# Performance work log

Hardware: AMD Instinct MI355X
Metric: run time of the kernel (lower is better)

## Reference

```python
import jax, jax.numpy as jnp
import numpy as np

H = 16  # num_attention_heads

def setup_inputs() -> dict:
    key = jax.random.key(0)
    ks = jax.random.split(key, 4)
    B, S, D = 4, 2048, 1024
    scale = 1.0 / np.sqrt(D)
    return {
        "hidden_states": jax.random.normal(ks[0], (B, S, D), dtype=jnp.float32),
        "attention_mask": jnp.zeros((B, 1, 1, S), dtype=jnp.float32),
        "Wq": jax.random.normal(ks[1], (D, D), dtype=jnp.float32) * scale,
        "bq": jnp.zeros((D,), dtype=jnp.float32),
        "Wk": jax.random.normal(ks[2], (D, D), dtype=jnp.float32) * scale,
        "bk": jnp.zeros((D,), dtype=jnp.float32),
        "Wv": jax.random.normal(ks[3], (D, D), dtype=jnp.float32) * scale,
        "bv": jnp.zeros((D,), dtype=jnp.float32),
    }

def _split_heads(x, B, S):
    # [B,S,D] -> [B,H,S,Dh]
    return x.reshape(B, S, H, -1).transpose(0, 2, 1, 3)

def reference(hidden_states, attention_mask, Wq, bq, Wk, bk, Wv, bv):
    B, S, D = hidden_states.shape
    Dh = D // H
    q = _split_heads(hidden_states @ Wq.T + bq, B, S)  # [B,H,S,Dh]
    k = _split_heads(hidden_states @ Wk.T + bk, B, S)
    v = _split_heads(hidden_states @ Wv.T + bv, B, S)
    scores = jnp.einsum("bhqd,bhkd->bhqk", q, k) / jnp.sqrt(jnp.float32(Dh))
    scores = scores + attention_mask  # additive mask, broadcast [B,1,1,S]
    probs = jax.nn.softmax(scores, axis=-1)  # dropout is identity in eval mode
    ctx = jnp.einsum("bhqk,bhkd->bhqd", probs, v)  # [B,H,S,Dh]
    ctx = ctx.transpose(0, 2, 1, 3).reshape(B, S, D)
    return ctx
```

## Files before the change

kernel.cpp:

```cpp
#include <hip/hip_runtime.h>
#include <hip/hip_bf16.h>
#include <stdint.h>

#define LOG2E 1.44269504088896340736f
#define SCL   (0.125f * LOG2E)

typedef __attribute__((ext_vector_type(8)))  short short8;
typedef __attribute__((ext_vector_type(4)))  float floatx4;
typedef __attribute__((ext_vector_type(16))) float floatx16;
typedef __attribute__((ext_vector_type(4)))  unsigned short ushort4v;

#define GLP(g, l)                                                              \
    __builtin_amdgcn_global_load_lds(                                          \
        (const __attribute__((address_space(1))) void*)(g),                    \
        (__attribute__((address_space(3))) void*)(l), 16, 0, 0)

#if __has_builtin(__builtin_amdgcn_exp2f)
#define EXP2(x) __builtin_amdgcn_exp2f(x)
#else
#define EXP2(x) exp2f(x)
#endif

static __device__ __forceinline__ unsigned short f2bf(float f) {
    union { float f; unsigned u; } v; v.f = f;
    unsigned r = v.u + 0x7FFFu + ((v.u >> 16) & 1u);
    return (unsigned short)(r >> 16);
}

static __device__ __forceinline__ unsigned pack2bf(float a, float b) {
    __hip_bfloat162 h = __float22bfloat162_rn(make_float2(a, b));
    union { __hip_bfloat162 h; unsigned u; } c; c.h = h; return c.u;
}

__global__ __launch_bounds__(256) void cvt_kernel(const float* __restrict__ in,
                                                  unsigned short* __restrict__ out,
                                                  int n4) {
    int i = blockIdx.x * 256 + threadIdx.x;
    if (i < n4) {
        float4 v = ((const float4*)in)[i];
        ushort4v o;
        o.x = f2bf(v.x); o.y = f2bf(v.y); o.z = f2bf(v.z); o.w = f2bf(v.w);
        ((ushort4v*)out)[i] = o;
    }
}

__global__ __launch_bounds__(256) void cvt_w3m(const float* __restrict__ Wq,
                                               const float* __restrict__ Wk,
                                               const float* __restrict__ Wv,
                                               const float* __restrict__ mask,
                                               unsigned short* __restrict__ out,
                                               float* __restrict__ maskl) {
    int i = blockIdx.x * 256 + threadIdx.x;
    if (i < 786432) {
        const float* src; int j;
        if (i < 262144)      { src = Wq; j = i; }
        else if (i < 524288) { src = Wk; j = i - 262144; }
        else                 { src = Wv; j = i - 524288; }
        float4 v = ((const float4*)src)[j];
        ushort4v o;
        o.x = f2bf(v.x); o.y = f2bf(v.y); o.z = f2bf(v.z); o.w = f2bf(v.w);
        ((ushort4v*)out)[i] = o;
    } else if (i < 786432 + 2048) {
        int j = i - 786432;
        float4 v = ((const float4*)mask)[j];
        ((float4*)maskl)[j] = make_float4(v.x * LOG2E, v.y * LOG2E,
                                          v.z * LOG2E, v.w * LOG2E);
    }
}

__global__ __launch_bounds__(256) void qkv_gemm(
        const unsigned short* __restrict__ X,
        const unsigned short* __restrict__ W,
        const float* __restrict__ bq, const float* __restrict__ bk,
        const float* __restrict__ bv,
        unsigned short* __restrict__ Qf,
        unsigned short* __restrict__ Kf,
        unsigned short* __restrict__ Vt)
{
    __shared__ __align__(16) unsigned short sh[17408];
    unsigned short* Ash = sh;
    unsigned short* Bsh = sh + 8192;

    const int tid  = threadIdx.x;
    const int lane = tid & 63;
    const int wv   = tid >> 6;
    const int quad = lane >> 4;
    const int ln   = lane & 15;
    const int mBase = blockIdx.x * 128;
    const int nBase = blockIdx.y * 128;
    const int wm = (wv >> 1) * 64;
    const int wn = (wv & 1) * 64;

    floatx4 acc[4][4];
#pragma unroll
    for (int i = 0; i < 4; ++i)
#pragma unroll
        for (int j = 0; j < 4; ++j) acc[i][j] = 0.0f;

    const int sr = lane >> 3;
    const int kc = (lane & 7) ^ sr;

    for (int kb = 0; kb < 1024; kb += 64) {
        __syncthreads();
#pragma unroll
        for (int s = 0; s < 4; ++s) {
            const int seg = wv * 4 + s;
            const int row = seg * 8 + sr;
            GLP(X + (size_t)(mBase + row) * 1024 + kb + kc * 8, Ash + seg * 512);
            GLP(W + (size_t)(nBase + row) * 1024 + kb + kc * 8, Bsh + seg * 512);
        }
        __syncthreads();
#pragma unroll
        for (int kk = 0; kk < 2; ++kk) {
            const int c = kk * 4 + quad;
            short8 aF[4], bF[4];
#pragma unroll
            for (int i = 0; i < 4; ++i) {
                const int R = wm + i * 16 + ln;
                aF[i] = *(const short8*)(Ash + (R >> 3) * 512 + (R & 7) * 64 + ((c ^ (R & 7)) * 8));
            }
#pragma unroll
            for (int j = 0; j < 4; ++j) {
                const int R = wn + j * 16 + ln;
                bF[j] = *(const short8*)(Bsh + (R >> 3) * 512 + (R & 7) * 64 + ((c ^ (R & 7)) * 8));
            }
#pragma unroll
            for (int i = 0; i < 4; ++i)
#pragma unroll
                for (int j = 0; j < 4; ++j)
                    acc[i][j] = __builtin_amdgcn_mfma_f32_16x16x32_bf16(
                        aF[i], bF[j], acc[i][j], 0, 0, 0);
        }
    }

    if (blockIdx.y < 16) {
        unsigned short* dst = (blockIdx.y < 8) ? Qf : Kf;
        const float* bias   = (blockIdx.y < 8) ? bq : bk;
        const int nb = nBase & 1023;
        float bj[4];
#pragma unroll
        for (int j = 0; j < 4; ++j)
            bj[j] = bias[nb + wn + j * 16 + ln];
        __syncthreads();
#pragma unroll
        for (int j = 0; j < 4; ++j) {
            const int col = wn + j * 16 + ln;
#pragma unroll
            for (int i = 0; i < 4; ++i) {
                const int row0 = wm + i * 16 + quad * 4;
#pragma unroll
                for (int r = 0; r < 4; ++r)
                    sh[(row0 + r) * 136 + col] = f2bf(acc[i][j][r] + bj[j]);
            }
        }
        __syncthreads();
#pragma unroll
        for (int it = 0; it < 8; ++it) {
            const int row  = it * 16 + (tid >> 4);
            const int part = tid & 15;
            short8 v = *(const short8*)(sh + row * 136 + part * 8);
            *(short8*)(dst + (size_t)(mBase + row) * 1024 + nb + part * 8) = v;
        }
    } else {
#pragma unroll
        for (int j = 0; j < 4; ++j) {
            const int gn = nBase + wn + j * 16 + ln;
            const int c  = gn & 1023;
            const int h  = c >> 6;
            const int d  = c & 63;
            const float bias = bv[c];
#pragma unroll
            for (int i = 0; i < 4; ++i) {
                const int gm0 = mBase + wm + i * 16 + quad * 4;
                const int b   = gm0 >> 11;
                const int s0  = gm0 & 2047;
                ushort4v pv;
#pragma unroll
                for (int r = 0; r < 4; ++r) pv[r] = f2bf(acc[i][j][r] + bias);
                *(ushort4v*)(Vt + (size_t)((b * 16 + h) * 64 + d) * 2048 + s0) = pv;
            }
        }
    }
}

__global__ __launch_bounds__(256) void attn_kernel(
        const unsigned short* __restrict__ Qf,
        const unsigned short* __restrict__ Kf,
        const unsigned short* __restrict__ VT,
        const float* __restrict__ maskl,
        float* __restrict__ out)
{
    __shared__ __align__(16) unsigned short Ksh[128 * 64];
    __shared__ __align__(16) unsigned short Vsh[64 * 128];
    __shared__ __align__(16) unsigned short Psh[4 * 32 * 64];
    __shared__ __align__(16) float Msh[128];

    const int tid  = threadIdx.x;
    const int lane = tid & 63;
    const int wv   = tid >> 6;
    const int q32  = lane & 31;
    const int hi   = lane >> 5;
    const int bh   = blockIdx.x & 63;
    const int qt   = blockIdx.x >> 6;
    const int b    = bh >> 4;
    const int h    = bh & 15;
    const int q0   = qt * 128 + wv * 32;
    const int sw   = q32 & 7;

    short8 bQ[4];
#pragma unroll
    for (int ks = 0; ks < 4; ++ks)
        bQ[ks] = *(const short8*)(Qf + (size_t)(b * 2048 + q0 + q32) * 1024
                                     + h * 64 + ks * 16 + hi * 8);
    short8 ones;
#pragma unroll
    for (int j = 0; j < 8; ++j) ones[j] = (short)0x3F80;

    floatx16 accO0 = 0.0f, accO1 = 0.0f, accL = 0.0f;

    const unsigned short* gK = Kf + (size_t)(b * 2048) * 1024 + h * 64;
    const unsigned short* gV = VT + (size_t)(bh * 64) * 2048;
    const float* mrow = maskl + b * 2048;
    unsigned short* pw = Psh + wv * (32 * 64);

    const int krr = lane >> 3;
    const int kcs = lane & 7;
    const int vrr = lane >> 4;
    const int vcs = lane & 15;

    for (int kb = 0; kb < 2048; kb += 128) {
        __syncthreads();
#pragma unroll
        for (int s = 0; s < 4; ++s) {
            const int seg = wv * 4 + s;
            const int rK  = seg * 8 + krr;
            const int cK  = kcs ^ (rK & 7);
            GLP(gK + (size_t)(kb + rK) * 1024 + cK * 8, Ksh + seg * 512);
            const int rV  = seg * 4 + vrr;
            const int cV  = vcs ^ (rV & 7);
            GLP(gV + (size_t)rV * 2048 + kb + cV * 8, Vsh + seg * 512);
        }
        if (tid < 32) GLP(mrow + kb + lane * 4, Msh);
        __syncthreads();

#pragma unroll
        for (int half = 0; half < 2; ++half) {
#pragma unroll
            for (int mt = 0; mt < 2; ++mt) {
                floatx16 sacc = 0.0f;
#pragma unroll
                for (int ks = 0; ks < 4; ++ks) {
                    const int row  = half * 64 + mt * 32 + q32;
                    const int slot = (2 * ks + hi) ^ sw;
                    short8 aK = *(const short8*)(Ksh + row * 64 + slot * 8);
                    sacc = __builtin_amdgcn_mfma_f32_32x32x16_bf16(aK, bQ[ks], sacc, 0, 0, 0);
                }
#pragma unroll
                for (int g = 0; g < 4; ++g) {
                    const int key0 = mt * 32 + g * 8 + hi * 4;
                    float4 mv4 = *(const float4*)(Msh + half * 64 + key0);
                    float p0 = EXP2(sacc[g * 4 + 0] * SCL + mv4.x);
                    float p1 = EXP2(sacc[g * 4 + 1] * SCL + mv4.y);
                    float p2 = EXP2(sacc[g * 4 + 2] * SCL + mv4.z);
                    float p3 = EXP2(sacc[g * 4 + 3] * SCL + mv4.w);
                    *(uint2*)(pw + q32 * 64 + (((mt * 4 + g) ^ sw) * 8) + hi * 4) =
                        make_uint2(pack2bf(p0, p1), pack2bf(p2, p3));
                }
            }

#pragma unroll
            for (int ks = 0; ks < 4; ++ks) {
                const int cs = (2 * ks + hi) ^ sw;
                short8 aP  = *(const short8*)(pw + q32 * 64 + cs * 8);
                const int cv = half * 8 + cs;
                short8 bV0 = *(const short8*)(Vsh + q32 * 128 + cv * 8);
                short8 bV1 = *(const short8*)(Vsh + (32 + q32) * 128 + cv * 8);
                accO0 = __builtin_amdgcn_mfma_f32_32x32x16_bf16(aP, bV0, accO0, 0, 0, 0);
                accO1 = __builtin_amdgcn_mfma_f32_32x32x16_bf16(aP, bV1, accO1, 0, 0, 0);
                accL  = __builtin_amdgcn_mfma_f32_32x32x16_bf16(aP, ones, accL, 0, 0, 0);
            }
        }
    }

#pragma unroll
    for (int g = 0; g < 4; ++g)
#pragma unroll
        for (int rr = 0; rr < 4; ++rr) {
            const int r   = g * 4 + rr;
            const int row = rr + 8 * g + 4 * hi;
            const float linv = 1.0f / accL[r];
            float* op = out + (size_t)(b * 2048 + q0 + row) * 1024 + h * 64 + q32;
            op[0]  = accO0[r] * linv;
            op[32] = accO1[r] * linv;
        }
}

extern "C" void kernel_launch(void* const* d_in, const int* in_sizes, int n_in,
                              void* d_out, int out_size, void* d_ws, size_t ws_size,
                              hipStream_t stream) {
    const float* X    = (const float*)d_in[0];
    const float* mask = (const float*)d_in[1];
    const float* Wq   = (const float*)d_in[2];
    const float* bq   = (const float*)d_in[3];
    const float* Wk   = (const float*)d_in[4];
    const float* bk   = (const float*)d_in[5];
    const float* Wv   = (const float*)d_in[6];
    const float* bv   = (const float*)d_in[7];
    float* out = (float*)d_out;

    char* ws = (char*)d_ws;
    unsigned short* xb  = (unsigned short*)(ws);
    unsigned short* wb  = (unsigned short*)(ws + 16777216);
    unsigned short* qf  = (unsigned short*)(ws + 23068672);
    unsigned short* kf  = (unsigned short*)(ws + 39845888);
    unsigned short* vtb = (unsigned short*)(ws + 56623104);
    float*          ml  = (float*)(ws + 73400320);

    cvt_kernel<<<8192, 256, 0, stream>>>(X, xb, 2097152);
    cvt_w3m<<<3080, 256, 0, stream>>>(Wq, Wk, Wv, mask, wb, ml);

    qkv_gemm<<<dim3(64, 24), 256, 0, stream>>>(xb, wb, bq, bk, bv, qf, kf, vtb);

    attn_kernel<<<1024, 256, 0, stream>>>(qf, kf, vtb, ml, out);
}
```

Measured before the change: 272.8 us.

## Keep softmax probabilities in registers via lane shuffles and sum row totals in VALU

The attention kernel no longer stages the bf16 probability tile through shared memory. It builds the MFMA A operand for the PV product directly from the score accumulator registers, using cross-half-wave shuffles. The row-sum MFMA against a ones vector is replaced by a scalar per-lane accumulation that is reduced at the end and passed through a small shared buffer. Launch bounds now request 4 blocks per CU to raise occupancy, which may force register pressure or spills. The row sum is now accumulated in fp32 before bf16 rounding, so it can differ slightly from the bf16-weighted numerator.

```diff
diff --git a/kernel.cpp b/kernel.cpp
--- a/kernel.cpp
+++ b/kernel.cpp
@@ -183,7 +183,7 @@
     }
 }
 
-__global__ __launch_bounds__(256) void attn_kernel(
+__global__ __launch_bounds__(256, 4) void attn_kernel(
         const unsigned short* __restrict__ Qf,
         const unsigned short* __restrict__ Kf,
         const unsigned short* __restrict__ VT,
@@ -192,8 +192,8 @@
 {
     __shared__ __align__(16) unsigned short Ksh[128 * 64];
     __shared__ __align__(16) unsigned short Vsh[64 * 128];
-    __shared__ __align__(16) unsigned short Psh[4 * 32 * 64];
     __shared__ __align__(16) float Msh[128];
+    __shared__ __align__(16) float Lsh[128];
 
     const int tid  = threadIdx.x;
     const int lane = tid & 63;
@@ -212,16 +212,13 @@
     for (int ks = 0; ks < 4; ++ks)
         bQ[ks] = *(const short8*)(Qf + (size_t)(b * 2048 + q0 + q32) * 1024
                                      + h * 64 + ks * 16 + hi * 8);
-    short8 ones;
-#pragma unroll
-    for (int j = 0; j < 8; ++j) ones[j] = (short)0x3F80;
-
-    floatx16 accO0 = 0.0f, accO1 = 0.0f, accL = 0.0f;
+
+    floatx16 accO0 = 0.0f, accO1 = 0.0f;
+    float l_c = 0.0f;
 
     const unsigned short* gK = Kf + (size_t)(b * 2048) * 1024 + h * 64;
     const unsigned short* gV = VT + (size_t)(bh * 64) * 2048;
     const float* mrow = maskl + b * 2048;
-    unsigned short* pw = Psh + wv * (32 * 64);
 
     const int krr = lane >> 3;
     const int kcs = lane & 7;
@@ -255,44 +252,56 @@
                     short8 aK = *(const short8*)(Ksh + row * 64 + slot * 8);
                     sacc = __builtin_amdgcn_mfma_f32_32x32x16_bf16(aK, bQ[ks], sacc, 0, 0, 0);
                 }
-#pragma unroll
-                for (int g = 0; g < 4; ++g) {
-                    const int key0 = mt * 32 + g * 8 + hi * 4;
-                    float4 mv4 = *(const float4*)(Msh + half * 64 + key0);
-                    float p0 = EXP2(sacc[g * 4 + 0] * SCL + mv4.x);
-                    float p1 = EXP2(sacc[g * 4 + 1] * SCL + mv4.y);
-                    float p2 = EXP2(sacc[g * 4 + 2] * SCL + mv4.z);
-                    float p3 = EXP2(sacc[g * 4 + 3] * SCL + mv4.w);
-                    *(uint2*)(pw + q32 * 64 + (((mt * 4 + g) ^ sw) * 8) + hi * 4) =
-                        make_uint2(pack2bf(p0, p1), pack2bf(p2, p3));
+                unsigned u0[4], u1[4], e0[4], e1[4];
+#pragma unroll
+                for (int a = 0; a < 4; ++a) {
+                    const int key0 = half * 64 + mt * 32 + a * 8 + hi * 4;
+                    float4 mv4 = *(const float4*)(Msh + key0);
+                    float p0 = EXP2(sacc[a * 4 + 0] * SCL + mv4.x);
+                    float p1 = EXP2(sacc[a * 4 + 1] * SCL + mv4.y);
+                    float p2 = EXP2(sacc[a * 4 + 2] * SCL + mv4.z);
+                    float p3 = EXP2(sacc[a * 4 + 3] * SCL + mv4.w);
+                    l_c += (p0 + p1) + (p2 + p3);
+                    u0[a] = pack2bf(p0, p1);
+                    u1[a] = pack2bf(p2, p3);
+                    e0[a] = (unsigned)__shfl_xor((int)u0[a], 32, 64);
+                    e1[a] = (unsigned)__shfl_xor((int)u1[a], 32, 64);
                 }
-            }
-
-#pragma unroll
-            for (int ks = 0; ks < 4; ++ks) {
-                const int cs = (2 * ks + hi) ^ sw;
-                short8 aP  = *(const short8*)(pw + q32 * 64 + cs * 8);
-                const int cv = half * 8 + cs;
-                short8 bV0 = *(const short8*)(Vsh + q32 * 128 + cv * 8);
-                short8 bV1 = *(const short8*)(Vsh + (32 + q32) * 128 + cv * 8);
-                accO0 = __builtin_amdgcn_mfma_f32_32x32x16_bf16(aP, bV0, accO0, 0, 0, 0);
-                accO1 = __builtin_amdgcn_mfma_f32_32x32x16_bf16(aP, bV1, accO1, 0, 0, 0);
-                accL  = __builtin_amdgcn_mfma_f32_32x32x16_bf16(aP, ones, accL, 0, 0, 0);
-            }
-        }
-    }
-
-#pragma unroll
-    for (int g = 0; g < 4; ++g)
+#pragma unroll
+                for (int ks2 = 0; ks2 < 2; ++ks2) {
+                    const int a0 = ks2 * 2;
+                    union { unsigned u[4]; short8 s; } aP;
+                    aP.u[0] = hi ? e0[a0 + 1] : u0[a0];
+                    aP.u[1] = hi ? e1[a0 + 1] : u1[a0];
+                    aP.u[2] = hi ? u0[a0 + 1] : e0[a0];
+                    aP.u[3] = hi ? u1[a0 + 1] : e1[a0];
+                    const int ks = mt * 2 + ks2;
+                    const int cv = half * 8 + ((2 * ks + hi) ^ sw);
+                    short8 bV0 = *(const short8*)(Vsh + q32 * 128 + cv * 8);
+                    short8 bV1 = *(const short8*)(Vsh + (32 + q32) * 128 + cv * 8);
+                    accO0 = __builtin_amdgcn_mfma_f32_32x32x16_bf16(aP.s, bV0, accO0, 0, 0, 0);
+                    accO1 = __builtin_amdgcn_mfma_f32_32x32x16_bf16(aP.s, bV1, accO1, 0, 0, 0);
+                }
+            }
+        }
+    }
+
+    l_c += __shfl_xor(l_c, 32, 64);
+    if (lane < 32) Lsh[wv * 32 + q32] = 1.0f / l_c;
+#pragma unroll
+    for (int g = 0; g < 4; ++g) {
+        float4 inv4 = *(const float4*)(Lsh + wv * 32 + g * 8 + hi * 4);
 #pragma unroll
         for (int rr = 0; rr < 4; ++rr) {
             const int r   = g * 4 + rr;
             const int row = rr + 8 * g + 4 * hi;
-            const float linv = 1.0f / accL[r];
+            const float linv = (rr == 0) ? inv4.x : (rr == 1) ? inv4.y
+                             : (rr == 2) ? inv4.z : inv4.w;
             float* op = out + (size_t)(b * 2048 + q0 + row) * 1024 + h * 64 + q32;
             op[0]  = accO0[r] * linv;
             op[32] = accO1[r] * linv;
         }
+    }
 }
 
 extern "C" void kernel_launch(void* const* d_in, const int* in_sizes, int n_in,
```

Measured after the change: 263.1 us. -3.6%, faster.
